# Kernel tuning notes

Measured on AMD Instinct MI355X. Metric: run time of the kernel, lower is better.

Reference implementation:

```python
import jax, jax.numpy as jnp
import numpy as np

EMBED_DIM = 1024
VOCAB = 32000
B, S = 4, 4096


def setup_inputs() -> dict:
    key = jax.random.key(0)
    ks = jax.random.split(key, 6)
    scale = 1.0 / np.sqrt(EMBED_DIM)
    x = jax.random.randint(ks[0], (B, S), 0, VOCAB, dtype=jnp.int64)
    embed = jax.random.normal(ks[1], (VOCAB, EMBED_DIM), dtype=jnp.float32)
    qkv_w = jax.random.normal(ks[2], (EMBED_DIM, 3 * EMBED_DIM), dtype=jnp.float32) * scale
    qkv_b = jnp.zeros((3 * EMBED_DIM,), dtype=jnp.float32)
    out_w = jax.random.normal(ks[3], (EMBED_DIM, VOCAB), dtype=jnp.float32) * scale
    out_b = jnp.zeros((VOCAB,), dtype=jnp.float32)
    return {"x": x, "embed": embed, "qkv_w": qkv_w, "qkv_b": qkv_b,
            "out_w": out_w, "out_b": out_b}


def reference(x, embed, qkv_w, qkv_b, out_w, out_b):
    h = embed[x]                                   # [B,S,D] token embedding lookup
    qkv = h @ qkv_w + qkv_b                        # [B,S,3D]
    qkv = qkv.reshape(B, S, 3, EMBED_DIM)
    q, k, v = qkv[:, :, 0], qkv[:, :, 1], qkv[:, :, 2]
    logits = jnp.einsum('bqd,bkd->bqk', q, k) / jnp.sqrt(jnp.float32(EMBED_DIM))
    attn = jax.nn.softmax(logits, axis=-1)         # [B,S,S] full score matrix (as in source)
    out = jnp.einsum('bqk,bkd->bqd', attn, v)
    h = out + h                                    # residual
    # source applies output projection then slices last token; equivalent to
    # projecting the last-token hidden only.
    return h[:, -1, :] @ out_w + out_b             # [B, vocab]
```

## Files before the change

### kernel.cpp

```cpp
#include <hip/hip_runtime.h>
#include <hip/hip_bf16.h>

typedef __bf16 bf16;
typedef __bf16 bf16x4 __attribute__((ext_vector_type(4)));
typedef __bf16 bf16x8 __attribute__((ext_vector_type(8)));
typedef float floatx4 __attribute__((ext_vector_type(4)));

#define EMBED 1024
#define VOCAB 32000
#define BB    4
#define SS    4096
#define NTOK  (BB * SS)
#define NKV   2048

__device__ __forceinline__ void async_copy16(void* lds, const void* g) {
    __builtin_amdgcn_global_load_lds(
        (const __attribute__((address_space(1))) unsigned int*)g,
        (__attribute__((address_space(3))) unsigned int*)lds, 16, 0, 0);
}

__global__ void gather_embed(const int* __restrict__ x,
                             const float* __restrict__ embed,
                             bf16* __restrict__ h,
                             float* __restrict__ h_last,
                             float* __restrict__ h_final) {
    int t = blockIdx.x;
    int tid = threadIdx.x;
    int row = x[t];
    const float4* src = (const float4*)(embed + (size_t)row * EMBED);
    float4 v = src[tid];
    bf16x4 o; o.x = (bf16)v.x; o.y = (bf16)v.y; o.z = (bf16)v.z; o.w = (bf16)v.w;
    *(bf16x4*)(h + (size_t)t * EMBED + tid * 4) = o;
    if ((t & (SS - 1)) == SS - 1) {
        int b = t >> 12;
        *(float4*)(h_last  + b * EMBED + tid * 4) = v;
        *(float4*)(h_final + b * EMBED + tid * 4) = v;
    }
}

__global__ void init_qout(const float* __restrict__ qkv_b,
                          const float* __restrict__ out_b,
                          float* __restrict__ q, float* __restrict__ out) {
    int i = blockIdx.x * 256 + threadIdx.x;
    if (i < BB * VOCAB) {
        out[i] = out_b[i % VOCAB];
    } else if (i < BB * VOCAB + BB * EMBED) {
        int k = i - BB * VOCAB;
        q[k] = qkv_b[k & (EMBED - 1)];
    }
}

__global__ void wkvt_transpose(const float* __restrict__ qkv_w,
                               bf16* __restrict__ WkvT) {
    __shared__ float T[32][33];
    int n0 = blockIdx.x * 32, d0 = blockIdx.y * 32;
    int tid = threadIdx.x;
    int c = tid & 31, r = tid >> 5;
#pragma unroll
    for (int i = 0; i < 4; ++i) {
        int d = r + i * 8;
        T[c][d] = qkv_w[(size_t)(d0 + d) * (3 * EMBED) + EMBED + n0 + c];
    }
    __syncthreads();
#pragma unroll
    for (int i = 0; i < 4; ++i) {
        int n = r + i * 8;
        WkvT[(size_t)(n0 + n) * EMBED + d0 + c] = (bf16)T[n][c];
    }
}

__global__ void q_gemm(const float* __restrict__ h_last,
                       const float* __restrict__ qkv_w,
                       float* __restrict__ q) {
    __shared__ float hs[BB * 256];
    int tid = threadIdx.x;
    int j = blockIdx.x * 256 + tid;
    int d0 = blockIdx.y * 256;
    for (int i = tid; i < BB * 256; i += 256)
        hs[i] = h_last[(i >> 8) * EMBED + d0 + (i & 255)];
    __syncthreads();
    float a0 = 0, a1 = 0, a2 = 0, a3 = 0;
#pragma unroll 4
    for (int dd = 0; dd < 256; ++dd) {
        float wv = qkv_w[(size_t)(d0 + dd) * (3 * EMBED) + j];
        a0 += hs[dd] * wv; a1 += hs[256 + dd] * wv;
        a2 += hs[512 + dd] * wv; a3 += hs[768 + dd] * wv;
    }
    atomicAdd(q + j, a0);
    atomicAdd(q + EMBED + j, a1);
    atomicAdd(q + 2 * EMBED + j, a2);
    atomicAdd(q + 3 * EMBED + j, a3);
}

__global__ __launch_bounds__(256, 2) void gemm_kv(
    const bf16* __restrict__ A,
    const bf16* __restrict__ BT,
    const float* __restrict__ bias,
    bf16* __restrict__ C) {
    __shared__ bf16 As[128 * 32];
    __shared__ bf16 Bs[128 * 32];
    const int K = EMBED;
    int tid = threadIdx.x;
    int wave = tid >> 6, lane = tid & 63;
    int wm = wave >> 1, wn = wave & 1;
    int quad = lane >> 4, l16 = lane & 15;

    floatx4 acc[4][4];
#pragma unroll
    for (int a = 0; a < 4; ++a)
#pragma unroll
        for (int b = 0; b < 4; ++b) acc[a][b] = (floatx4)0.0f;

    const bf16* Abase = A + (size_t)blockIdx.x * 128 * K;
    const bf16* Bbase = BT + (size_t)blockIdx.y * 128 * K;

    for (int k0 = 0; k0 < K; k0 += 32) {
        __syncthreads();
#pragma unroll
        for (int i = 0; i < 2; ++i) {
            int c = wave * 128 + i * 64 + lane;
            int row = c >> 2, ko = (c & 3) * 8;
            async_copy16(As + c * 8, Abase + (size_t)row * K + k0 + ko);
            async_copy16(Bs + c * 8, Bbase + (size_t)row * K + k0 + ko);
        }
        __syncthreads();
        bf16x8 af[4], bfr[4];
#pragma unroll
        for (int mt = 0; mt < 4; ++mt)
            af[mt] = *(const bf16x8*)(As + (wm * 64 + mt * 16 + l16) * 32 + quad * 8);
#pragma unroll
        for (int nt = 0; nt < 4; ++nt)
            bfr[nt] = *(const bf16x8*)(Bs + (wn * 64 + nt * 16 + l16) * 32 + quad * 8);
#pragma unroll
        for (int mt = 0; mt < 4; ++mt)
#pragma unroll
            for (int nt = 0; nt < 4; ++nt)
                acc[mt][nt] = __builtin_amdgcn_mfma_f32_16x16x32_bf16(
                    af[mt], bfr[nt], acc[mt][nt], 0, 0, 0);
    }

    int crow0 = blockIdx.x * 128 + wm * 64;
    int ccol0 = blockIdx.y * 128 + wn * 64;
#pragma unroll
    for (int mt = 0; mt < 4; ++mt)
#pragma unroll
        for (int nt = 0; nt < 4; ++nt) {
            int col = ccol0 + nt * 16 + l16;
            float bs = bias[col];
#pragma unroll
            for (int r = 0; r < 4; ++r) {
                int row = crow0 + mt * 16 + quad * 4 + r;
                C[(size_t)row * NKV + col] = (bf16)(acc[mt][nt][r] + bs);
            }
        }
}

__global__ void attn_logits(const bf16* __restrict__ KV,
                            const float* __restrict__ q,
                            float* __restrict__ logits) {
    int gw = blockIdx.x * 4 + (threadIdx.x >> 6);
    int b = gw >> 12, t = gw & (SS - 1);
    int lane = threadIdx.x & 63;
    const bf16* Krow = KV + (size_t)(b * SS + t) * NKV;
    const float* qb = q + b * EMBED;
    float sum = 0.0f;
#pragma unroll
    for (int i = 0; i < 2; ++i) {
        int d0 = i * 512 + lane * 8;
        bf16x8 kv8 = *(const bf16x8*)(Krow + d0);
        float4 qa = *(const float4*)(qb + d0);
        float4 qc = *(const float4*)(qb + d0 + 4);
        sum += qa.x * (float)kv8[0] + qa.y * (float)kv8[1] +
               qa.z * (float)kv8[2] + qa.w * (float)kv8[3] +
               qc.x * (float)kv8[4] + qc.y * (float)kv8[5] +
               qc.z * (float)kv8[6] + qc.w * (float)kv8[7];
    }
#pragma unroll
    for (int o = 32; o; o >>= 1) sum += __shfl_down(sum, o);
    if (lane == 0) logits[gw] = sum * 0.03125f;
}

__global__ void softmax_k(const float* __restrict__ logits,
                          float* __restrict__ wts) {
    int b = blockIdx.x, tid = threadIdx.x;
    const float* l = logits + b * SS;
    __shared__ float redm[4], reds[4];
    float m = -1e30f;
    for (int i = tid; i < SS; i += 256) m = fmaxf(m, l[i]);
#pragma unroll
    for (int o = 32; o; o >>= 1) m = fmaxf(m, __shfl_down(m, o));
    if ((tid & 63) == 0) redm[tid >> 6] = m;
    __syncthreads();
    m = fmaxf(fmaxf(redm[0], redm[1]), fmaxf(redm[2], redm[3]));
    float s = 0.0f;
    for (int i = tid; i < SS; i += 256) s += expf(l[i] - m);
#pragma unroll
    for (int o = 32; o; o >>= 1) s += __shfl_down(s, o);
    if ((tid & 63) == 0) reds[tid >> 6] = s;
    __syncthreads();
    s = reds[0] + reds[1] + reds[2] + reds[3];
    float inv = 1.0f / s;
    for (int i = tid; i < SS; i += 256) wts[b * SS + i] = expf(l[i] - m) * inv;
}

__global__ void attn_av(const bf16* __restrict__ KV,
                        const float* __restrict__ wts,
                        float* __restrict__ h_final) {
    int bx = blockIdx.x;
    int b = bx >> 6, dc = (bx >> 4) & 3, ts = bx & 15;
    int tid = threadIdx.x;
    int d = dc * 256 + tid;
    const bf16* Vb = KV + (size_t)(b * SS + ts * 256) * NKV + EMBED + d;
    const float* wb = wts + b * SS + ts * 256;
    float acc = 0.0f;
#pragma unroll 8
    for (int j = 0; j < 256; ++j)
        acc += wb[j] * (float)Vb[(size_t)j * NKV];
    atomicAdd(h_final + b * EMBED + d, acc);
}

__global__ void out_gemm(const float* __restrict__ h_final,
                         const float* __restrict__ out_w,
                         float* __restrict__ out) {
    __shared__ float hs[BB * 256];
    int tid = threadIdx.x;
    int j = blockIdx.x * 256 + tid;
    int d0 = blockIdx.y * 256;
    for (int i = tid; i < BB * 256; i += 256)
        hs[i] = h_final[(i >> 8) * EMBED + d0 + (i & 255)];
    __syncthreads();
    float a0 = 0, a1 = 0, a2 = 0, a3 = 0;
#pragma unroll 4
    for (int dd = 0; dd < 256; ++dd) {
        float wv = out_w[(size_t)(d0 + dd) * VOCAB + j];
        a0 += hs[dd] * wv; a1 += hs[256 + dd] * wv;
        a2 += hs[512 + dd] * wv; a3 += hs[768 + dd] * wv;
    }
    atomicAdd(out + j, a0);
    atomicAdd(out + VOCAB + j, a1);
    atomicAdd(out + 2 * VOCAB + j, a2);
    atomicAdd(out + 3 * VOCAB + j, a3);
}

extern "C" void kernel_launch(void* const* d_in, const int* in_sizes, int n_in,
                              void* d_out, int out_size, void* d_ws, size_t ws_size,
                              hipStream_t stream) {
    const int*   x      = (const int*)d_in[0];
    const float* embed  = (const float*)d_in[1];
    const float* qkv_w  = (const float*)d_in[2];
    const float* qkv_b  = (const float*)d_in[3];
    const float* out_w  = (const float*)d_in[4];
    const float* out_b  = (const float*)d_in[5];
    float* out = (float*)d_out;

    char* ws = (char*)d_ws;
    bf16*  h       = (bf16*)(ws);
    bf16*  KV      = (bf16*)(ws + 33554432);
    bf16*  WkvT    = (bf16*)(ws + 100663296);
    float* h_last  = (float*)(ws + 104857600);
    float* h_final = (float*)(ws + 104873984);
    float* q       = (float*)(ws + 104890368);
    float* logits  = (float*)(ws + 104906752);
    float* wts     = (float*)(ws + 104972288);

    gather_embed<<<NTOK, 256, 0, stream>>>(x, embed, h, h_last, h_final);
    init_qout<<<(BB * VOCAB + BB * EMBED + 255) / 256, 256, 0, stream>>>(
        qkv_b, out_b, q, out);
    wkvt_transpose<<<dim3(64, 32), 256, 0, stream>>>(qkv_w, WkvT);
    q_gemm<<<dim3(4, 4), 256, 0, stream>>>(h_last, qkv_w, q);
    gemm_kv<<<dim3(NTOK / 128, NKV / 128), 256, 0, stream>>>(
        h, WkvT, qkv_b + EMBED, KV);
    attn_logits<<<SS, 256, 0, stream>>>(KV, q, logits);
    softmax_k<<<BB, 256, 0, stream>>>(logits, wts);
    attn_av<<<256, 256, 0, stream>>>(KV, wts, h_final);
    out_gemm<<<dim3(VOCAB / 256, 4), 256, 0, stream>>>(h_final, out_w, out);
}
```

Before: 433.4 us.

## Replace atomic split-K GEMVs with partial buffers and reduction, retile attention kernels

The q and output projection GEMVs now split K into 16 segments that write partial sums to a workspace buffer, followed by separate reduce kernels that add the bias. This replaces the atomic accumulation and the init kernel. Attention logits stage q in shared memory. Softmax uses 1024 threads and keeps values in registers instead of reading logits three times. attn_av is re-tiled to 64-token chunks with 4-wide bf16 loads. The changes add two launches and reuse the h buffer region for output partials.

```diff
diff --git a/kernel.cpp b/kernel.cpp
--- a/kernel.cpp
+++ b/kernel.cpp
@@ -12,6 +12,7 @@
 #define SS    4096
 #define NTOK  (BB * SS)
 #define NKV   2048
+#define NSEG  16
 
 __device__ __forceinline__ void async_copy16(void* lds, const void* g) {
     __builtin_amdgcn_global_load_lds(
@@ -38,18 +39,6 @@
     }
 }
 
-__global__ void init_qout(const float* __restrict__ qkv_b,
-                          const float* __restrict__ out_b,
-                          float* __restrict__ q, float* __restrict__ out) {
-    int i = blockIdx.x * 256 + threadIdx.x;
-    if (i < BB * VOCAB) {
-        out[i] = out_b[i % VOCAB];
-    } else if (i < BB * VOCAB + BB * EMBED) {
-        int k = i - BB * VOCAB;
-        q[k] = qkv_b[k & (EMBED - 1)];
-    }
-}
-
 __global__ void wkvt_transpose(const float* __restrict__ qkv_w,
                                bf16* __restrict__ WkvT) {
     __shared__ float T[32][33];
@@ -71,25 +60,40 @@
 
 __global__ void q_gemm(const float* __restrict__ h_last,
                        const float* __restrict__ qkv_w,
-                       float* __restrict__ q) {
-    __shared__ float hs[BB * 256];
-    int tid = threadIdx.x;
-    int j = blockIdx.x * 256 + tid;
-    int d0 = blockIdx.y * 256;
-    for (int i = tid; i < BB * 256; i += 256)
-        hs[i] = h_last[(i >> 8) * EMBED + d0 + (i & 255)];
-    __syncthreads();
-    float a0 = 0, a1 = 0, a2 = 0, a3 = 0;
+                       float* __restrict__ qpart) {
+    __shared__ float hs[BB * 64];
+    int tid = threadIdx.x;
+    int seg = blockIdx.x, d0 = seg * 64;
+    hs[tid] = h_last[(tid >> 6) * EMBED + d0 + (tid & 63)];
+    __syncthreads();
+    int j0 = tid * 4;
+    floatx4 acc[BB];
+#pragma unroll
+    for (int b = 0; b < BB; ++b) acc[b] = (floatx4)0.0f;
 #pragma unroll 4
-    for (int dd = 0; dd < 256; ++dd) {
-        float wv = qkv_w[(size_t)(d0 + dd) * (3 * EMBED) + j];
-        a0 += hs[dd] * wv; a1 += hs[256 + dd] * wv;
-        a2 += hs[512 + dd] * wv; a3 += hs[768 + dd] * wv;
-    }
-    atomicAdd(q + j, a0);
-    atomicAdd(q + EMBED + j, a1);
-    atomicAdd(q + 2 * EMBED + j, a2);
-    atomicAdd(q + 3 * EMBED + j, a3);
+    for (int dd = 0; dd < 64; ++dd) {
+        float4 w = *(const float4*)(qkv_w + (size_t)(d0 + dd) * (3 * EMBED) + j0);
+#pragma unroll
+        for (int b = 0; b < BB; ++b) {
+            float hv = hs[b * 64 + dd];
+            acc[b][0] += hv * w.x; acc[b][1] += hv * w.y;
+            acc[b][2] += hv * w.z; acc[b][3] += hv * w.w;
+        }
+    }
+#pragma unroll
+    for (int b = 0; b < BB; ++b)
+        *(floatx4*)(qpart + ((size_t)seg * BB + b) * EMBED + j0) = acc[b];
+}
+
+__global__ void q_reduce(const float* __restrict__ qpart,
+                         const float* __restrict__ qkv_b,
+                         float* __restrict__ q) {
+    int k = blockIdx.x * 256 + threadIdx.x;
+    int b = k >> 10, d = k & (EMBED - 1);
+    float s = qkv_b[d];
+#pragma unroll
+    for (int sg = 0; sg < NSEG; ++sg) s += qpart[((size_t)sg * BB + b) * EMBED + d];
+    q[k] = s;
 }
 
 __global__ __launch_bounds__(256, 2) void gemm_kv(
@@ -158,18 +162,20 @@
 __global__ void attn_logits(const bf16* __restrict__ KV,
                             const float* __restrict__ q,
                             float* __restrict__ logits) {
-    int gw = blockIdx.x * 4 + (threadIdx.x >> 6);
-    int b = gw >> 12, t = gw & (SS - 1);
+    __shared__ float qs[EMBED];
+    int b = blockIdx.x >> 10;
+    int t = (blockIdx.x & 1023) * 4 + (threadIdx.x >> 6);
     int lane = threadIdx.x & 63;
+    *(float4*)(qs + threadIdx.x * 4) = *(const float4*)(q + b * EMBED + threadIdx.x * 4);
+    __syncthreads();
     const bf16* Krow = KV + (size_t)(b * SS + t) * NKV;
-    const float* qb = q + b * EMBED;
     float sum = 0.0f;
 #pragma unroll
     for (int i = 0; i < 2; ++i) {
         int d0 = i * 512 + lane * 8;
         bf16x8 kv8 = *(const bf16x8*)(Krow + d0);
-        float4 qa = *(const float4*)(qb + d0);
-        float4 qc = *(const float4*)(qb + d0 + 4);
+        float4 qa = *(const float4*)(qs + d0);
+        float4 qc = *(const float4*)(qs + d0 + 4);
         sum += qa.x * (float)kv8[0] + qa.y * (float)kv8[1] +
                qa.z * (float)kv8[2] + qa.w * (float)kv8[3] +
                qc.x * (float)kv8[4] + qc.y * (float)kv8[5] +
@@ -177,69 +183,100 @@
     }
 #pragma unroll
     for (int o = 32; o; o >>= 1) sum += __shfl_down(sum, o);
-    if (lane == 0) logits[gw] = sum * 0.03125f;
+    if (lane == 0) logits[b * SS + t] = sum * 0.03125f;
 }
 
 __global__ void softmax_k(const float* __restrict__ logits,
                           float* __restrict__ wts) {
     int b = blockIdx.x, tid = threadIdx.x;
+    __shared__ float redm[16], reds[16];
     const float* l = logits + b * SS;
-    __shared__ float redm[4], reds[4];
-    float m = -1e30f;
-    for (int i = tid; i < SS; i += 256) m = fmaxf(m, l[i]);
+    float x0 = l[tid], x1 = l[tid + 1024], x2 = l[tid + 2048], x3 = l[tid + 3072];
+    float m = fmaxf(fmaxf(x0, x1), fmaxf(x2, x3));
 #pragma unroll
     for (int o = 32; o; o >>= 1) m = fmaxf(m, __shfl_down(m, o));
     if ((tid & 63) == 0) redm[tid >> 6] = m;
     __syncthreads();
-    m = fmaxf(fmaxf(redm[0], redm[1]), fmaxf(redm[2], redm[3]));
-    float s = 0.0f;
-    for (int i = tid; i < SS; i += 256) s += expf(l[i] - m);
+    float M = redm[0];
+#pragma unroll
+    for (int i = 1; i < 16; ++i) M = fmaxf(M, redm[i]);
+    float e0 = expf(x0 - M), e1 = expf(x1 - M), e2 = expf(x2 - M), e3 = expf(x3 - M);
+    float s = e0 + e1 + e2 + e3;
 #pragma unroll
     for (int o = 32; o; o >>= 1) s += __shfl_down(s, o);
     if ((tid & 63) == 0) reds[tid >> 6] = s;
     __syncthreads();
-    s = reds[0] + reds[1] + reds[2] + reds[3];
-    float inv = 1.0f / s;
-    for (int i = tid; i < SS; i += 256) wts[b * SS + i] = expf(l[i] - m) * inv;
+    float S = 0.0f;
+#pragma unroll
+    for (int i = 0; i < 16; ++i) S += reds[i];
+    float inv = 1.0f / S;
+    float* w = wts + b * SS;
+    w[tid] = e0 * inv; w[tid + 1024] = e1 * inv;
+    w[tid + 2048] = e2 * inv; w[tid + 3072] = e3 * inv;
 }
 
 __global__ void attn_av(const bf16* __restrict__ KV,
                         const float* __restrict__ wts,
                         float* __restrict__ h_final) {
-    int bx = blockIdx.x;
-    int b = bx >> 6, dc = (bx >> 4) & 3, ts = bx & 15;
-    int tid = threadIdx.x;
-    int d = dc * 256 + tid;
-    const bf16* Vb = KV + (size_t)(b * SS + ts * 256) * NKV + EMBED + d;
-    const float* wb = wts + b * SS + ts * 256;
-    float acc = 0.0f;
-#pragma unroll 8
-    for (int j = 0; j < 256; ++j)
-        acc += wb[j] * (float)Vb[(size_t)j * NKV];
-    atomicAdd(h_final + b * EMBED + d, acc);
+    int b = blockIdx.x >> 6, ts = blockIdx.x & 63;
+    int tid = threadIdx.x;
+    __shared__ float wsh[64];
+    if (tid < 64) wsh[tid] = wts[b * SS + ts * 64 + tid];
+    __syncthreads();
+    int d = tid * 4;
+    const bf16* Vb = KV + (size_t)(b * SS + ts * 64) * NKV + EMBED + d;
+    float a0 = 0, a1 = 0, a2 = 0, a3 = 0;
+#pragma unroll 4
+    for (int j = 0; j < 64; ++j) {
+        bf16x4 v = *(const bf16x4*)(Vb + (size_t)j * NKV);
+        float w = wsh[j];
+        a0 += w * (float)v.x; a1 += w * (float)v.y;
+        a2 += w * (float)v.z; a3 += w * (float)v.w;
+    }
+    atomicAdd(h_final + b * EMBED + d + 0, a0);
+    atomicAdd(h_final + b * EMBED + d + 1, a1);
+    atomicAdd(h_final + b * EMBED + d + 2, a2);
+    atomicAdd(h_final + b * EMBED + d + 3, a3);
 }
 
 __global__ void out_gemm(const float* __restrict__ h_final,
                          const float* __restrict__ out_w,
-                         float* __restrict__ out) {
-    __shared__ float hs[BB * 256];
-    int tid = threadIdx.x;
-    int j = blockIdx.x * 256 + tid;
-    int d0 = blockIdx.y * 256;
-    for (int i = tid; i < BB * 256; i += 256)
-        hs[i] = h_final[(i >> 8) * EMBED + d0 + (i & 255)];
-    __syncthreads();
-    float a0 = 0, a1 = 0, a2 = 0, a3 = 0;
+                         float* __restrict__ opart) {
+    __shared__ float hs[BB * 64];
+    int tid = threadIdx.x;
+    int seg = blockIdx.y, d0 = seg * 64;
+    hs[tid] = h_final[(tid >> 6) * EMBED + d0 + (tid & 63)];
+    __syncthreads();
+    int j0 = blockIdx.x * 1024 + tid * 4;
+    if (j0 >= VOCAB) return;
+    floatx4 acc[BB];
+#pragma unroll
+    for (int b = 0; b < BB; ++b) acc[b] = (floatx4)0.0f;
 #pragma unroll 4
-    for (int dd = 0; dd < 256; ++dd) {
-        float wv = out_w[(size_t)(d0 + dd) * VOCAB + j];
-        a0 += hs[dd] * wv; a1 += hs[256 + dd] * wv;
-        a2 += hs[512 + dd] * wv; a3 += hs[768 + dd] * wv;
-    }
-    atomicAdd(out + j, a0);
-    atomicAdd(out + VOCAB + j, a1);
-    atomicAdd(out + 2 * VOCAB + j, a2);
-    atomicAdd(out + 3 * VOCAB + j, a3);
+    for (int dd = 0; dd < 64; ++dd) {
+        float4 w = *(const float4*)(out_w + (size_t)(d0 + dd) * VOCAB + j0);
+#pragma unroll
+        for (int b = 0; b < BB; ++b) {
+            float hv = hs[b * 64 + dd];
+            acc[b][0] += hv * w.x; acc[b][1] += hv * w.y;
+            acc[b][2] += hv * w.z; acc[b][3] += hv * w.w;
+        }
+    }
+#pragma unroll
+    for (int b = 0; b < BB; ++b)
+        *(floatx4*)(opart + ((size_t)seg * BB + b) * VOCAB + j0) = acc[b];
+}
+
+__global__ void out_reduce(const float* __restrict__ opart,
+                           const float* __restrict__ out_b,
+                           float* __restrict__ out) {
+    int i = blockIdx.x * 256 + threadIdx.x;
+    if (i >= BB * VOCAB) return;
+    int b = i / VOCAB, j = i - b * VOCAB;
+    float s = out_b[j];
+#pragma unroll
+    for (int sg = 0; sg < NSEG; ++sg) s += opart[((size_t)sg * BB + b) * VOCAB + j];
+    out[i] = s;
 }
 
 extern "C" void kernel_launch(void* const* d_in, const int* in_sizes, int n_in,
@@ -255,6 +292,7 @@
 
     char* ws = (char*)d_ws;
     bf16*  h       = (bf16*)(ws);
+    float* opart   = (float*)(ws);
     bf16*  KV      = (bf16*)(ws + 33554432);
     bf16*  WkvT    = (bf16*)(ws + 100663296);
     float* h_last  = (float*)(ws + 104857600);
@@ -262,16 +300,17 @@
     float* q       = (float*)(ws + 104890368);
     float* logits  = (float*)(ws + 104906752);
     float* wts     = (float*)(ws + 104972288);
+    float* qpart   = (float*)(ws + 105037824);
 
     gather_embed<<<NTOK, 256, 0, stream>>>(x, embed, h, h_last, h_final);
-    init_qout<<<(BB * VOCAB + BB * EMBED + 255) / 256, 256, 0, stream>>>(
-        qkv_b, out_b, q, out);
     wkvt_transpose<<<dim3(64, 32), 256, 0, stream>>>(qkv_w, WkvT);
-    q_gemm<<<dim3(4, 4), 256, 0, stream>>>(h_last, qkv_w, q);
+    q_gemm<<<NSEG, 256, 0, stream>>>(h_last, qkv_w, qpart);
+    q_reduce<<<16, 256, 0, stream>>>(qpart, qkv_b, q);
     gemm_kv<<<dim3(NTOK / 128, NKV / 128), 256, 0, stream>>>(
         h, WkvT, qkv_b + EMBED, KV);
     attn_logits<<<SS, 256, 0, stream>>>(KV, q, logits);
-    softmax_k<<<BB, 256, 0, stream>>>(logits, wts);
+    softmax_k<<<BB, 1024, 0, stream>>>(logits, wts);
     attn_av<<<256, 256, 0, stream>>>(KV, wts, h_final);
-    out_gemm<<<dim3(VOCAB / 256, 4), 256, 0, stream>>>(h_final, out_w, out);
-}
+    out_gemm<<<dim3(32, NSEG), 256, 0, stream>>>(h_final, out_w, opart);
+    out_reduce<<<(BB * VOCAB + 255) / 256, 256, 0, stream>>>(opart, out_b, out);
+}
```

After: 397.3 us. 8.3% less time.
